# Optimization experiments

Hardware: AMD Instinct MI355X
Metric: run time of the kernel (lower is better)

The kernel has to match this reference:

```python
import jax, jax.numpy as jnp
import numpy as np

B, S, H = 2, 2048, 1024          # batch, seq, hidden_size
I = 512                          # expert_ffn_hidden_size
E_R, E_Z = 32, 8                 # routed experts, zero (identity) experts
E_T = E_R + E_Z                  # total experts
K = 6                            # moe_topk
SCALE = 2.5                      # routed_scaling_factor
W_INIT = 0.02


def setup_inputs() -> dict:
    key = jax.random.key(0)
    k0, k1, k2, k3 = jax.random.split(key, 4)
    return {
        "hidden_states": jax.random.normal(k0, (B, S, H), jnp.float32),
        "classifier_weight": jax.random.normal(k1, (E_T, H), jnp.float32) * W_INIT,
        "e_score_correction_bias": jnp.zeros((E_T,), jnp.float32),
        "gate_up_proj": jax.random.normal(k2, (E_T, 2 * I, H), jnp.float32) * W_INIT,
        "down_proj": jax.random.normal(k3, (E_R, H, I), jnp.float32) * W_INIT,
    }


def reference(hidden_states, classifier_weight, e_score_correction_bias,
              gate_up_proj, down_proj):
    orig_shape = hidden_states.shape
    x = hidden_states.reshape(-1, H).astype(jnp.float32)      # [T, H]
    T = x.shape[0]

    # ---- router (fp32 like the torch code) ----
    logits = x @ classifier_weight.T                          # [T, E_T]
    scores = jax.nn.softmax(logits, axis=-1)
    _, topk_idx = jax.lax.top_k(scores + e_score_correction_bias[None, :], K)
    topk_w = jnp.take_along_axis(scores, topk_idx, axis=1) * SCALE  # [T, K]

    # dense per-(token, expert) combine weights; 0 for unselected experts
    w_full = jnp.zeros((T, E_T), jnp.float32).at[
        jnp.arange(T)[:, None], topk_idx].add(topk_w)          # [T, E_T]

    # zero experts: weighted identity
    zero_w = w_full[:, E_R:].sum(axis=-1, keepdims=True)       # [T, 1]
    out0 = x * zero_w

    # routed experts: SwiGLU MLP per expert, scanned over experts
    routed_w = w_full[:, :E_R].T                               # [E_R, T]

    def body(out, xs):
        Wgu, Wd, we = xs                                       # [2I,H],[H,I],[T]
        gate, up = jnp.split(x @ Wgu.T, 2, axis=-1)            # [T, I] each
        y = (jax.nn.silu(gate) * up) @ Wd.T                    # [T, H]
        return out + we[:, None] * y, None

    out, _ = jax.lax.scan(body, out0, (gate_up_proj[:E_R], down_proj, routed_w))
    return out.reshape(orig_shape).astype(hidden_states.dtype)
```

## Files before the change

### kernel.cpp

```cpp
#include <hip/hip_runtime.h>
#include <float.h>
#include <math.h>

#define TT 4096
#define HH 1024
#define II 512
#define E_R 32
#define E_T 40
#define TOPK 6
#define SCALE_F 2.5f

typedef __bf16 bf16x8 __attribute__((ext_vector_type(8)));
typedef float f32x4 __attribute__((ext_vector_type(4)));

__device__ inline unsigned short f2bf(float f) {
  unsigned int u = __builtin_bit_cast(unsigned int, f);
  unsigned int r = (u + 0x7FFFu + ((u >> 16) & 1u)) >> 16;
  return (unsigned short)r;
}

__device__ inline uint4 cvt8(float4 a, float4 b) {
  uint4 v;
  v.x = (unsigned)f2bf(a.x) | ((unsigned)f2bf(a.y) << 16);
  v.y = (unsigned)f2bf(a.z) | ((unsigned)f2bf(a.w) << 16);
  v.z = (unsigned)f2bf(b.x) | ((unsigned)f2bf(b.y) << 16);
  v.w = (unsigned)f2bf(b.z) | ((unsigned)f2bf(b.w) << 16);
  return v;
}

__device__ inline void lds_store16(unsigned short* base, int row, int c8, uint4 v) {
  int byte = (row * 128 + c8 * 16) ^ ((row & 7) << 4);
  *reinterpret_cast<uint4*>(reinterpret_cast<char*>(base) + byte) = v;
}
__device__ inline bf16x8 lds_frag(const unsigned short* base, int row, int kb) {
  int byte = (row * 128 + kb * 2) ^ ((row & 7) << 4);
  uint4 v = *reinterpret_cast<const uint4*>(reinterpret_cast<const char*>(base) + byte);
  return __builtin_bit_cast(bf16x8, v);
}

__device__ inline f32x4 mfma16(bf16x8 a, bf16x8 b, f32x4 c) {
  return __builtin_amdgcn_mfma_f32_16x16x32_bf16(a, b, c, 0, 0, 0);
}

__global__ void k_convert_x(const float* __restrict__ x, unsigned short* __restrict__ xb) {
  int i = blockIdx.x * 256 + threadIdx.x;
  const float4* p = reinterpret_cast<const float4*>(x) + (size_t)i * 2;
  float4 a = p[0], b = p[1];
  reinterpret_cast<uint4*>(xb)[i] = cvt8(a, b);
}

__global__ __launch_bounds__(256) void k_logits(const float* __restrict__ x,
                                                const float* __restrict__ wcls,
                                                float* __restrict__ logits) {
  __shared__ float4 ws4[E_T * 64];
  const int tid = threadIdx.x;
  const int lane = tid & 63;
  const int wave = tid >> 6;
  const int token = blockIdx.x * 4 + wave;
  const float4* x4 = reinterpret_cast<const float4*>(x);
  const float4* w4 = reinterpret_cast<const float4*>(wcls);

  float acc[E_T];
  #pragma unroll
  for (int e = 0; e < E_T; ++e) acc[e] = 0.f;

  for (int c = 0; c < 4; ++c) {
    if (c) __syncthreads();
    #pragma unroll
    for (int j = 0; j < 10; ++j) {
      int v = tid + j * 256;
      int e = v >> 6, kq = v & 63;
      ws4[v] = w4[e * 256 + c * 64 + kq];
    }
    float4 xv = x4[(size_t)token * 256 + c * 64 + lane];
    __syncthreads();
    #pragma unroll
    for (int e = 0; e < E_T; ++e) {
      float4 w = ws4[e * 64 + lane];
      acc[e] += xv.x * w.x + xv.y * w.y + xv.z * w.z + xv.w * w.w;
    }
  }

  float mine = 0.f;
  #pragma unroll
  for (int e = 0; e < E_T; ++e) {
    float r = acc[e];
    #pragma unroll
    for (int o = 32; o; o >>= 1) r += __shfl_xor(r, o);
    if (lane == e) mine = r;
  }
  if (lane < E_T) logits[(size_t)token * E_T + lane] = mine;
}

__global__ void k_topk(const float* __restrict__ logits, const float* __restrict__ bias,
                       float* __restrict__ zero_w, int* __restrict__ counts,
                       int* __restrict__ tok_list, float* __restrict__ wt_list) {
  int t = blockIdx.x * 64 + threadIdx.x;
  float l[E_T];
  const float4* lp = reinterpret_cast<const float4*>(logits + (size_t)t * E_T);
  #pragma unroll
  for (int j = 0; j < E_T / 4; ++j) {
    float4 v = lp[j];
    l[j * 4 + 0] = v.x; l[j * 4 + 1] = v.y; l[j * 4 + 2] = v.z; l[j * 4 + 3] = v.w;
  }
  float m = -FLT_MAX;
  #pragma unroll
  for (int e = 0; e < E_T; ++e) m = fmaxf(m, l[e]);
  float den = 0.f;
  #pragma unroll
  for (int e = 0; e < E_T; ++e) { l[e] = __expf(l[e] - m); den += l[e]; }
  float inv = 1.f / den;
  float sel[E_T];
  #pragma unroll
  for (int e = 0; e < E_T; ++e) { l[e] *= inv; sel[e] = l[e] + bias[e]; }

  unsigned long long used = 0ull;
  float zw = 0.f;
  for (int k = 0; k < TOPK; ++k) {
    float bv = -FLT_MAX; int bj = 0;
    #pragma unroll
    for (int e = 0; e < E_T; ++e) {
      float v = ((used >> e) & 1ull) ? -FLT_MAX : sel[e];
      if (v > bv) { bv = v; bj = e; }
    }
    used |= 1ull << bj;
    float wgt = (bv - bias[bj]) * SCALE_F;
    if (bj >= E_R) {
      zw += wgt;
    } else {
      int p = atomicAdd(&counts[bj], 1);
      tok_list[bj * TT + p] = t;
      wt_list[bj * TT + p] = wgt;
    }
  }
  zero_w[t] = zw;
}

__global__ void k_scan(const int* __restrict__ counts, int* __restrict__ offsets) {
  if (threadIdx.x == 0) {
    int s = 0;
    for (int e = 0; e < E_R; ++e) { offsets[e] = s; s += counts[e]; }
    offsets[E_R] = s;
  }
}

__global__ void k_init_out(const float* __restrict__ x, const float* __restrict__ zero_w,
                           float* __restrict__ out) {
  int i = blockIdx.x * 256 + threadIdx.x;
  int t = i >> 8;
  float zw = zero_w[t];
  float4 v = reinterpret_cast<const float4*>(x)[i];
  v.x *= zw; v.y *= zw; v.z *= zw; v.w *= zw;
  reinterpret_cast<float4*>(out)[i] = v;
}

__global__ __launch_bounds__(256) void k_gemm1(
    const unsigned short* __restrict__ xb, const float* __restrict__ gup,
    const int* __restrict__ tok_list, const int* __restrict__ counts,
    const int* __restrict__ offsets, unsigned short* __restrict__ inter) {
  const int e = blockIdx.z;
  const int cnt = counts[e];
  const int row0 = blockIdx.y * 64;
  if (row0 >= cnt) return;
  const int n0 = blockIdx.x * 64;
  const int off = offsets[e];
  const int tid = threadIdx.x;
  const int lane = tid & 63;
  const int wave = tid >> 6;
  const int wr = wave >> 1, wc = wave & 1;

  __shared__ __align__(16) unsigned short lA[64 * 64];
  __shared__ __align__(16) unsigned short lBg[64 * 64];
  __shared__ __align__(16) unsigned short lBu[64 * 64];
  __shared__ int toks[64];

  if (tid < 64) {
    int r = row0 + tid;
    toks[tid] = tok_list[e * TT + (r < cnt ? r : cnt - 1)];
  }
  __syncthreads();

  f32x4 accg[2][2] = {}; f32x4 accu[2][2] = {};

  for (int k0 = 0; k0 < HH; k0 += 64) {
    #pragma unroll
    for (int c = tid; c < 512; c += 256) {
      int row = c >> 3, c8 = c & 7;
      uint4 v = *reinterpret_cast<const uint4*>(xb + (size_t)toks[row] * HH + (k0 + c8 * 8));
      lds_store16(lA, row, c8, v);
      const float4* p = reinterpret_cast<const float4*>(
          gup + ((size_t)e * 1024 + (n0 + row)) * HH + (k0 + c8 * 8));
      lds_store16(lBg, row, c8, cvt8(p[0], p[1]));
      const float4* q = reinterpret_cast<const float4*>(
          gup + ((size_t)e * 1024 + (512 + n0 + row)) * HH + (k0 + c8 * 8));
      lds_store16(lBu, row, c8, cvt8(q[0], q[1]));
    }
    __syncthreads();
    #pragma unroll
    for (int ks = 0; ks < 2; ++ks) {
      int kb = ks * 32 + ((lane >> 4) << 3);
      bf16x8 a0 = lds_frag(lA, wr * 32 + (lane & 15), kb);
      bf16x8 a1 = lds_frag(lA, wr * 32 + 16 + (lane & 15), kb);
      bf16x8 g0 = lds_frag(lBg, wc * 32 + (lane & 15), kb);
      bf16x8 g1 = lds_frag(lBg, wc * 32 + 16 + (lane & 15), kb);
      bf16x8 u0 = lds_frag(lBu, wc * 32 + (lane & 15), kb);
      bf16x8 u1 = lds_frag(lBu, wc * 32 + 16 + (lane & 15), kb);
      accg[0][0] = mfma16(a0, g0, accg[0][0]);
      accg[0][1] = mfma16(a0, g1, accg[0][1]);
      accg[1][0] = mfma16(a1, g0, accg[1][0]);
      accg[1][1] = mfma16(a1, g1, accg[1][1]);
      accu[0][0] = mfma16(a0, u0, accu[0][0]);
      accu[0][1] = mfma16(a0, u1, accu[0][1]);
      accu[1][0] = mfma16(a1, u0, accu[1][0]);
      accu[1][1] = mfma16(a1, u1, accu[1][1]);
    }
    __syncthreads();
  }

  #pragma unroll
  for (int i = 0; i < 2; ++i)
    #pragma unroll
    for (int j = 0; j < 2; ++j)
      #pragma unroll
      for (int r = 0; r < 4; ++r) {
        int rloc = wr * 32 + i * 16 + ((lane >> 4) << 2) + r;
        int grow = row0 + rloc;
        if (grow < cnt) {
          int col = n0 + wc * 32 + j * 16 + (lane & 15);
          float g = accg[i][j][r], u = accu[i][j][r];
          float act = g * (1.f / (1.f + __expf(-g))) * u;
          inter[(size_t)(off + grow) * II + col] = f2bf(act);
        }
      }
}

__global__ __launch_bounds__(256) void k_gemm2(
    const unsigned short* __restrict__ inter, const float* __restrict__ dwn,
    const int* __restrict__ tok_list, const float* __restrict__ wt_list,
    const int* __restrict__ counts, const int* __restrict__ offsets,
    float* __restrict__ out) {
  const int e = blockIdx.z;
  const int cnt = counts[e];
  const int row0 = blockIdx.y * 64;
  if (row0 >= cnt) return;
  const int n0 = blockIdx.x * 64;
  const int off = offsets[e];
  const int tid = threadIdx.x;
  const int lane = tid & 63;
  const int wave = tid >> 6;
  const int wr = wave >> 1, wc = wave & 1;

  __shared__ __align__(16) unsigned short lA[64 * 64];
  __shared__ __align__(16) unsigned short lB[64 * 64];
  __shared__ int toks[64];
  __shared__ float wts[64];

  if (tid < 64) {
    int r = row0 + tid;
    int rc = r < cnt ? r : cnt - 1;
    toks[tid] = tok_list[e * TT + rc];
    wts[tid] = (r < cnt) ? wt_list[e * TT + rc] : 0.f;
  }
  __syncthreads();

  f32x4 acc[2][2] = {};

  for (int k0 = 0; k0 < II; k0 += 64) {
    #pragma unroll
    for (int c = tid; c < 512; c += 256) {
      int row = c >> 3, c8 = c & 7;
      int rr = row0 + row; rr = rr < cnt ? rr : cnt - 1;
      uint4 v = *reinterpret_cast<const uint4*>(inter + (size_t)(off + rr) * II + (k0 + c8 * 8));
      lds_store16(lA, row, c8, v);
      const float4* p = reinterpret_cast<const float4*>(
          dwn + ((size_t)e * HH + (n0 + row)) * II + (k0 + c8 * 8));
      lds_store16(lB, row, c8, cvt8(p[0], p[1]));
    }
    __syncthreads();
    #pragma unroll
    for (int ks = 0; ks < 2; ++ks) {
      int kb = ks * 32 + ((lane >> 4) << 3);
      bf16x8 a0 = lds_frag(lA, wr * 32 + (lane & 15), kb);
      bf16x8 a1 = lds_frag(lA, wr * 32 + 16 + (lane & 15), kb);
      bf16x8 b0 = lds_frag(lB, wc * 32 + (lane & 15), kb);
      bf16x8 b1 = lds_frag(lB, wc * 32 + 16 + (lane & 15), kb);
      acc[0][0] = mfma16(a0, b0, acc[0][0]);
      acc[0][1] = mfma16(a0, b1, acc[0][1]);
      acc[1][0] = mfma16(a1, b0, acc[1][0]);
      acc[1][1] = mfma16(a1, b1, acc[1][1]);
    }
    __syncthreads();
  }

  #pragma unroll
  for (int i = 0; i < 2; ++i)
    #pragma unroll
    for (int j = 0; j < 2; ++j)
      #pragma unroll
      for (int r = 0; r < 4; ++r) {
        int rloc = wr * 32 + i * 16 + ((lane >> 4) << 2) + r;
        int grow = row0 + rloc;
        if (grow < cnt) {
          int h = n0 + wc * 32 + j * 16 + (lane & 15);
          unsafeAtomicAdd(&out[(size_t)toks[rloc] * HH + h], acc[i][j][r] * wts[rloc]);
        }
      }
}


extern "C" void kernel_launch(void* const* d_in, const int* in_sizes, int n_in,
                              void* d_out, int out_size, void* d_ws, size_t ws_size,
                              hipStream_t stream) {
  const float* x    = (const float*)d_in[0];
  const float* wcls = (const float*)d_in[1];
  const float* bias = (const float*)d_in[2];
  const float* gup  = (const float*)d_in[3];
  const float* dwn  = (const float*)d_in[4];
  float* out = (float*)d_out;

  char* w = (char*)d_ws;
  unsigned short* xb   = (unsigned short*)(w + 0);
  float* zero_w        = (float*)(w + 8388608);
  int* counts          = (int*)(w + 8404992);
  int* offsets         = (int*)(w + 8405120);
  int* tok_list        = (int*)(w + 8405376);
  float* wt_list       = (float*)(w + 8929664);
  float* logits        = (float*)(w + 9453952);
  unsigned short* inter = (unsigned short*)(w + 10109312);

  hipMemsetAsync(counts, 0, E_R * sizeof(int), stream);
  k_convert_x<<<2048, 256, 0, stream>>>(x, xb);
  k_logits<<<1024, 256, 0, stream>>>(x, wcls, logits);
  k_topk<<<64, 64, 0, stream>>>(logits, bias, zero_w, counts, tok_list, wt_list);
  k_scan<<<1, 64, 0, stream>>>(counts, offsets);
  k_init_out<<<4096, 256, 0, stream>>>(x, zero_w, out);
  k_gemm1<<<dim3(8, 64, E_R), 256, 0, stream>>>(xb, gup, tok_list, counts, offsets, inter);
  k_gemm2<<<dim3(16, 64, E_R), 256, 0, stream>>>(inter, dwn, tok_list, wt_list, counts, offsets, out);
}
```

Measured before the change: 271.9 us.

## Enlarge expert GEMM tiles and load activations via direct global-to-LDS copies

Both grouped expert GEMMs now use 128-row token tiles, and the down-projection also uses 128-column tiles, so each converted fp32 weight tile is reused across more tokens and each wave holds more MFMA accumulators. The bf16 activation tiles are loaded with global_load_lds straight into swizzled shared memory, bypassing registers, and per-thread source addresses are precomputed outside the k loop. The bf16 conversion now uses native casts instead of manual rounding. The cost is more register and LDS pressure and fewer blocks, which may lower occupancy or leave partial tiles for experts with few tokens.

```diff
diff --git a/kernel.cpp b/kernel.cpp
--- a/kernel.cpp
+++ b/kernel.cpp
@@ -14,18 +14,21 @@
 typedef float f32x4 __attribute__((ext_vector_type(4)));
 
 __device__ inline unsigned short f2bf(float f) {
-  unsigned int u = __builtin_bit_cast(unsigned int, f);
-  unsigned int r = (u + 0x7FFFu + ((u >> 16) & 1u)) >> 16;
-  return (unsigned short)r;
+  __bf16 h = (__bf16)f;
+  return __builtin_bit_cast(unsigned short, h);
 }
 
 __device__ inline uint4 cvt8(float4 a, float4 b) {
-  uint4 v;
-  v.x = (unsigned)f2bf(a.x) | ((unsigned)f2bf(a.y) << 16);
-  v.y = (unsigned)f2bf(a.z) | ((unsigned)f2bf(a.w) << 16);
-  v.z = (unsigned)f2bf(b.x) | ((unsigned)f2bf(b.y) << 16);
-  v.w = (unsigned)f2bf(b.z) | ((unsigned)f2bf(b.w) << 16);
-  return v;
+  bf16x8 v;
+  v[0] = (__bf16)a.x; v[1] = (__bf16)a.y; v[2] = (__bf16)a.z; v[3] = (__bf16)a.w;
+  v[4] = (__bf16)b.x; v[5] = (__bf16)b.y; v[6] = (__bf16)b.z; v[7] = (__bf16)b.w;
+  return __builtin_bit_cast(uint4, v);
+}
+
+__device__ inline void gload_lds16(const void* g, void* l) {
+  __builtin_amdgcn_global_load_lds(
+      (__attribute__((address_space(1))) void*)g,
+      (__attribute__((address_space(3))) void*)l, 16, 0, 0);
 }
 
 __device__ inline void lds_store16(unsigned short* base, int row, int c8, uint4 v) {
@@ -160,7 +163,7 @@
     const int* __restrict__ offsets, unsigned short* __restrict__ inter) {
   const int e = blockIdx.z;
   const int cnt = counts[e];
-  const int row0 = blockIdx.y * 64;
+  const int row0 = blockIdx.y * 128;
   if (row0 >= cnt) return;
   const int n0 = blockIdx.x * 64;
   const int off = offsets[e];
@@ -169,66 +172,82 @@
   const int wave = tid >> 6;
   const int wr = wave >> 1, wc = wave & 1;
 
-  __shared__ __align__(16) unsigned short lA[64 * 64];
+  __shared__ __align__(16) unsigned short lA[128 * 64];
   __shared__ __align__(16) unsigned short lBg[64 * 64];
   __shared__ __align__(16) unsigned short lBu[64 * 64];
-  __shared__ int toks[64];
-
-  if (tid < 64) {
+  __shared__ int toks[128];
+
+  if (tid < 128) {
     int r = row0 + tid;
     toks[tid] = tok_list[e * TT + (r < cnt ? r : cnt - 1)];
   }
   __syncthreads();
 
-  f32x4 accg[2][2] = {}; f32x4 accu[2][2] = {};
+  size_t asrc[4];
+  #pragma unroll
+  for (int i = 0; i < 4; ++i) {
+    int lrow = wave * 32 + i * 8 + (lane >> 3);
+    asrc[i] = (size_t)toks[lrow] * HH + (((lane & 7) ^ (lrow & 7)) * 8);
+  }
+  const float4* bgp[2]; const float4* bup[2];
+  int brow[2], bc8[2];
+  #pragma unroll
+  for (int s = 0; s < 2; ++s) {
+    int idx = tid + s * 256;
+    brow[s] = idx >> 3; bc8[s] = idx & 7;
+    bgp[s] = reinterpret_cast<const float4*>(gup + ((size_t)e * 1024 + n0 + brow[s]) * HH) + bc8[s] * 2;
+    bup[s] = reinterpret_cast<const float4*>(gup + ((size_t)e * 1024 + 512 + n0 + brow[s]) * HH) + bc8[s] * 2;
+  }
+
+  f32x4 accg[4][2] = {}; f32x4 accu[4][2] = {};
 
   for (int k0 = 0; k0 < HH; k0 += 64) {
-    #pragma unroll
-    for (int c = tid; c < 512; c += 256) {
-      int row = c >> 3, c8 = c & 7;
-      uint4 v = *reinterpret_cast<const uint4*>(xb + (size_t)toks[row] * HH + (k0 + c8 * 8));
-      lds_store16(lA, row, c8, v);
-      const float4* p = reinterpret_cast<const float4*>(
-          gup + ((size_t)e * 1024 + (n0 + row)) * HH + (k0 + c8 * 8));
-      lds_store16(lBg, row, c8, cvt8(p[0], p[1]));
-      const float4* q = reinterpret_cast<const float4*>(
-          gup + ((size_t)e * 1024 + (512 + n0 + row)) * HH + (k0 + c8 * 8));
-      lds_store16(lBu, row, c8, cvt8(q[0], q[1]));
+    int kq = k0 >> 2;
+    #pragma unroll
+    for (int i = 0; i < 4; ++i)
+      gload_lds16(xb + asrc[i] + k0, lA + (wave * 32 + i * 8) * 64);
+    #pragma unroll
+    for (int s = 0; s < 2; ++s) {
+      float4 ga = bgp[s][kq], gb = bgp[s][kq + 1];
+      lds_store16(lBg, brow[s], bc8[s], cvt8(ga, gb));
+      float4 ua = bup[s][kq], ub = bup[s][kq + 1];
+      lds_store16(lBu, brow[s], bc8[s], cvt8(ua, ub));
     }
     __syncthreads();
     #pragma unroll
     for (int ks = 0; ks < 2; ++ks) {
       int kb = ks * 32 + ((lane >> 4) << 3);
-      bf16x8 a0 = lds_frag(lA, wr * 32 + (lane & 15), kb);
-      bf16x8 a1 = lds_frag(lA, wr * 32 + 16 + (lane & 15), kb);
-      bf16x8 g0 = lds_frag(lBg, wc * 32 + (lane & 15), kb);
-      bf16x8 g1 = lds_frag(lBg, wc * 32 + 16 + (lane & 15), kb);
-      bf16x8 u0 = lds_frag(lBu, wc * 32 + (lane & 15), kb);
-      bf16x8 u1 = lds_frag(lBu, wc * 32 + 16 + (lane & 15), kb);
-      accg[0][0] = mfma16(a0, g0, accg[0][0]);
-      accg[0][1] = mfma16(a0, g1, accg[0][1]);
-      accg[1][0] = mfma16(a1, g0, accg[1][0]);
-      accg[1][1] = mfma16(a1, g1, accg[1][1]);
-      accu[0][0] = mfma16(a0, u0, accu[0][0]);
-      accu[0][1] = mfma16(a0, u1, accu[0][1]);
-      accu[1][0] = mfma16(a1, u0, accu[1][0]);
-      accu[1][1] = mfma16(a1, u1, accu[1][1]);
-    }
-    __syncthreads();
-  }
-
-  #pragma unroll
-  for (int i = 0; i < 2; ++i)
+      bf16x8 a[4], g[2], u[2];
+      #pragma unroll
+      for (int i = 0; i < 4; ++i) a[i] = lds_frag(lA, wr * 64 + i * 16 + (lane & 15), kb);
+      #pragma unroll
+      for (int j = 0; j < 2; ++j) {
+        g[j] = lds_frag(lBg, wc * 32 + j * 16 + (lane & 15), kb);
+        u[j] = lds_frag(lBu, wc * 32 + j * 16 + (lane & 15), kb);
+      }
+      #pragma unroll
+      for (int i = 0; i < 4; ++i)
+        #pragma unroll
+        for (int j = 0; j < 2; ++j) {
+          accg[i][j] = mfma16(a[i], g[j], accg[i][j]);
+          accu[i][j] = mfma16(a[i], u[j], accu[i][j]);
+        }
+    }
+    __syncthreads();
+  }
+
+  #pragma unroll
+  for (int i = 0; i < 4; ++i)
     #pragma unroll
     for (int j = 0; j < 2; ++j)
       #pragma unroll
       for (int r = 0; r < 4; ++r) {
-        int rloc = wr * 32 + i * 16 + ((lane >> 4) << 2) + r;
+        int rloc = wr * 64 + i * 16 + ((lane >> 4) << 2) + r;
         int grow = row0 + rloc;
         if (grow < cnt) {
           int col = n0 + wc * 32 + j * 16 + (lane & 15);
-          float g = accg[i][j][r], u = accu[i][j][r];
-          float act = g * (1.f / (1.f + __expf(-g))) * u;
+          float gv = accg[i][j][r], uv = accu[i][j][r];
+          float act = gv / (1.f + __expf(-gv)) * uv;
           inter[(size_t)(off + grow) * II + col] = f2bf(act);
         }
       }
@@ -241,21 +260,21 @@
     float* __restrict__ out) {
   const int e = blockIdx.z;
   const int cnt = counts[e];
-  const int row0 = blockIdx.y * 64;
+  const int row0 = blockIdx.y * 128;
   if (row0 >= cnt) return;
-  const int n0 = blockIdx.x * 64;
+  const int h0 = blockIdx.x * 128;
   const int off = offsets[e];
   const int tid = threadIdx.x;
   const int lane = tid & 63;
   const int wave = tid >> 6;
   const int wr = wave >> 1, wc = wave & 1;
 
-  __shared__ __align__(16) unsigned short lA[64 * 64];
-  __shared__ __align__(16) unsigned short lB[64 * 64];
-  __shared__ int toks[64];
-  __shared__ float wts[64];
-
-  if (tid < 64) {
+  __shared__ __align__(16) unsigned short lA[128 * 64];
+  __shared__ __align__(16) unsigned short lB[128 * 64];
+  __shared__ int toks[128];
+  __shared__ float wts[128];
+
+  if (tid < 128) {
     int r = row0 + tid;
     int rc = r < cnt ? r : cnt - 1;
     toks[tid] = tok_list[e * TT + rc];
@@ -263,45 +282,62 @@
   }
   __syncthreads();
 
-  f32x4 acc[2][2] = {};
+  size_t asrc[4];
+  #pragma unroll
+  for (int i = 0; i < 4; ++i) {
+    int lrow = wave * 32 + i * 8 + (lane >> 3);
+    int rr = row0 + lrow; rr = rr < cnt ? rr : cnt - 1;
+    asrc[i] = (size_t)(off + rr) * II + (((lane & 7) ^ (lrow & 7)) * 8);
+  }
+  const float4* bp[4];
+  int brow[4], bc8[4];
+  #pragma unroll
+  for (int s = 0; s < 4; ++s) {
+    int idx = tid + s * 256;
+    brow[s] = idx >> 3; bc8[s] = idx & 7;
+    bp[s] = reinterpret_cast<const float4*>(dwn + ((size_t)e * HH + h0 + brow[s]) * II) + bc8[s] * 2;
+  }
+
+  f32x4 acc[4][4] = {};
 
   for (int k0 = 0; k0 < II; k0 += 64) {
-    #pragma unroll
-    for (int c = tid; c < 512; c += 256) {
-      int row = c >> 3, c8 = c & 7;
-      int rr = row0 + row; rr = rr < cnt ? rr : cnt - 1;
-      uint4 v = *reinterpret_cast<const uint4*>(inter + (size_t)(off + rr) * II + (k0 + c8 * 8));
-      lds_store16(lA, row, c8, v);
-      const float4* p = reinterpret_cast<const float4*>(
-          dwn + ((size_t)e * HH + (n0 + row)) * II + (k0 + c8 * 8));
-      lds_store16(lB, row, c8, cvt8(p[0], p[1]));
+    int kq = k0 >> 2;
+    #pragma unroll
+    for (int i = 0; i < 4; ++i)
+      gload_lds16(inter + asrc[i] + k0, lA + (wave * 32 + i * 8) * 64);
+    #pragma unroll
+    for (int s = 0; s < 4; ++s) {
+      float4 a = bp[s][kq], b = bp[s][kq + 1];
+      lds_store16(lB, brow[s], bc8[s], cvt8(a, b));
     }
     __syncthreads();
     #pragma unroll
     for (int ks = 0; ks < 2; ++ks) {
       int kb = ks * 32 + ((lane >> 4) << 3);
-      bf16x8 a0 = lds_frag(lA, wr * 32 + (lane & 15), kb);
-      bf16x8 a1 = lds_frag(lA, wr * 32 + 16 + (lane & 15), kb);
-      bf16x8 b0 = lds_frag(lB, wc * 32 + (lane & 15), kb);
-      bf16x8 b1 = lds_frag(lB, wc * 32 + 16 + (lane & 15), kb);
-      acc[0][0] = mfma16(a0, b0, acc[0][0]);
-      acc[0][1] = mfma16(a0, b1, acc[0][1]);
-      acc[1][0] = mfma16(a1, b0, acc[1][0]);
-      acc[1][1] = mfma16(a1, b1, acc[1][1]);
-    }
-    __syncthreads();
-  }
-
-  #pragma unroll
-  for (int i = 0; i < 2; ++i)
-    #pragma unroll
-    for (int j = 0; j < 2; ++j)
+      bf16x8 a[4], b[4];
+      #pragma unroll
+      for (int i = 0; i < 4; ++i) a[i] = lds_frag(lA, wr * 64 + i * 16 + (lane & 15), kb);
+      #pragma unroll
+      for (int j = 0; j < 4; ++j) b[j] = lds_frag(lB, wc * 64 + j * 16 + (lane & 15), kb);
+      #pragma unroll
+      for (int i = 0; i < 4; ++i)
+        #pragma unroll
+        for (int j = 0; j < 4; ++j)
+          acc[i][j] = mfma16(a[i], b[j], acc[i][j]);
+    }
+    __syncthreads();
+  }
+
+  #pragma unroll
+  for (int i = 0; i < 4; ++i)
+    #pragma unroll
+    for (int j = 0; j < 4; ++j)
       #pragma unroll
       for (int r = 0; r < 4; ++r) {
-        int rloc = wr * 32 + i * 16 + ((lane >> 4) << 2) + r;
+        int rloc = wr * 64 + i * 16 + ((lane >> 4) << 2) + r;
         int grow = row0 + rloc;
         if (grow < cnt) {
-          int h = n0 + wc * 32 + j * 16 + (lane & 15);
+          int h = h0 + wc * 64 + j * 16 + (lane & 15);
           unsafeAtomicAdd(&out[(size_t)toks[rloc] * HH + h], acc[i][j][r] * wts[rloc]);
         }
       }
@@ -334,6 +370,6 @@
   k_topk<<<64, 64, 0, stream>>>(logits, bias, zero_w, counts, tok_list, wt_list);
   k_scan<<<1, 64, 0, stream>>>(counts, offsets);
   k_init_out<<<4096, 256, 0, stream>>>(x, zero_w, out);
-  k_gemm1<<<dim3(8, 64, E_R), 256, 0, stream>>>(xb, gup, tok_list, counts, offsets, inter);
-  k_gemm2<<<dim3(16, 64, E_R), 256, 0, stream>>>(inter, dwn, tok_list, wt_list, counts, offsets, out);
-}
+  k_gemm1<<<dim3(8, 32, E_R), 256, 0, stream>>>(xb, gup, tok_list, counts, offsets, inter);
+  k_gemm2<<<dim3(8, 32, E_R), 256, 0, stream>>>(inter, dwn, tok_list, wt_list, counts, offsets, out);
+}
```

After: 307.7 us. 1.13x slower.
